# Kernel optimization log

Measured on AMD Instinct MI355X. Metric: run time of the kernel, lower is better.

## Reference

```python
import jax, jax.numpy as jnp
import numpy as np

B, N, C = 8192, 4, 768          # B = batch*tokens, N = n_streams, C = dim
HID = 4 * C                      # FFN hidden
EPS_RMS = 1.1920929e-7           # torch.finfo(float32).eps (nn.RMSNorm default eps=None)
EPS_SK = 1e-6                    # sinkhorn eps
SK_ITERS = 20
ALPHA = 0.01


def setup_inputs() -> dict:
    key = jax.random.key(0)
    ks = jax.random.split(key, 7)
    w = lambda k, shape: (jax.random.normal(k, shape, jnp.float32) * 0.02)
    return {
        "x": jax.random.normal(ks[0], (B, N, C), jnp.float32),
        "norm_w": jnp.ones((N * C,), jnp.float32),
        "w_pre": w(ks[1], (N, N * C)),
        "b_pre": jnp.zeros((N,), jnp.float32),
        "w_post": w(ks[2], (N, N * C)),
        "b_post": jnp.zeros((N,), jnp.float32),
        "w_res": w(ks[3], (N * N, N * C)),
        "b_res": jnp.zeros((N * N,), jnp.float32),
        "alpha_pre": jnp.array(ALPHA, jnp.float32),
        "alpha_post": jnp.array(ALPHA, jnp.float32),
        "alpha_res": jnp.array(ALPHA, jnp.float32),
        "w1": w(ks[4], (HID, C)),   # torch Linear weight layout [out, in]
        "b1": jnp.zeros((HID,), jnp.float32),
        "w2": w(ks[5], (C, HID)),
        "b2": jnp.zeros((C,), jnp.float32),
    }


def sinkhorn_knopp(logits):
    # logits: [B, n, n] -> doubly-stochastic matrix via 20 row/col normalizations
    M0 = jnp.exp(logits)

    def body(_, M):
        M = M / (M.sum(axis=-1, keepdims=True) + EPS_SK)
        M = M / (M.sum(axis=-2, keepdims=True) + EPS_SK)
        return M

    return jax.lax.fori_loop(0, SK_ITERS, body, M0)


def reference(x, norm_w, w_pre, b_pre, w_post, b_post, w_res, b_res,
              alpha_pre, alpha_post, alpha_res, w1, b1, w2, b2):
    b, n, c = x.shape
    x_flat = x.reshape(b, n * c)
    # RMSNorm over flattened streams
    x_norm = x_flat * jax.lax.rsqrt(jnp.mean(x_flat * x_flat, axis=-1, keepdims=True) + EPS_RMS) * norm_w
    # gate logits
    pre = alpha_pre * (x_norm @ w_pre.T) + b_pre            # [B, n]
    post = alpha_post * (x_norm @ w_post.T) + b_post        # [B, n]
    res_logits = (alpha_res * (x_norm @ w_res.T) + b_res).reshape(b, n, n)
    H_pre = jax.nn.sigmoid(pre)
    H_post = 2.0 * jax.nn.sigmoid(post)
    H_res = sinkhorn_knopp(res_logits)                      # [B, n, n]
    # pre-gate + stream mixing
    x_pre = x * H_pre[..., None]                            # [B, n, C]
    x_streams = jnp.einsum('bij,bjc->bic', H_res, x_pre)
    # fn = FFN applied on [B*n, C]
    h = jax.nn.gelu(x_streams.reshape(b * n, c) @ w1.T + b1, approximate=False)
    y = (h @ w2.T + b2).reshape(b, n, c)
    y = y * H_post[..., None]
    # residual mixed by the same DSM
    res = jnp.einsum('bij,bjc->bic', H_res, x)
    return res + y
```

## Files before the change

### kernel.cpp

```cpp
#include <hip/hip_runtime.h>

#define EPS_RMS 1.1920929e-7f
#define EPS_SK  1e-6f

typedef __bf16 bf16;
typedef __bf16 bf16x4 __attribute__((ext_vector_type(4)));
typedef __bf16 bf16x8 __attribute__((ext_vector_type(8)));
typedef float  f32x4  __attribute__((ext_vector_type(4)));

typedef __attribute__((address_space(3))) void lds_void;
typedef __attribute__((address_space(1))) void glb_void;

__device__ __forceinline__ void async_copy16(void* lds_dst, const void* gsrc) {
  __builtin_amdgcn_global_load_lds((glb_void*)gsrc, (lds_void*)lds_dst, 16, 0, 0);
}

__device__ __forceinline__ void wait_vmcnt0() {
  asm volatile("s_waitcnt vmcnt(0)" ::: "memory");
}

__device__ __forceinline__ void xcd_swizzle(int& bx, int& by) {
  const int gx = gridDim.x, nwg = gx * gridDim.y;
  const int flat = blockIdx.y * gx + blockIdx.x;
  const int q = nwg >> 3, r = nwg & 7;
  const int xcd = flat & 7, i = flat >> 3;
  const int lin = (xcd < r ? xcd * (q + 1) : r * (q + 1) + (xcd - r) * q) + i;
  bx = lin % gx;
  by = lin / gx;
}

__global__ __launch_bounds__(256) void convert_w_kernel(
    const float* __restrict__ w1, const float* __restrict__ w2,
    bf16* __restrict__ w1b, bf16* __restrict__ w2b) {
  size_t i = ((size_t)blockIdx.x * 256 + threadIdx.x) * 4;
  f32x4 a = *(const f32x4*)(w1 + i);
  f32x4 b = *(const f32x4*)(w2 + i);
  bf16x4 ab, bb;
#pragma unroll
  for (int q = 0; q < 4; ++q) { ab[q] = (bf16)a[q]; bb[q] = (bf16)b[q]; }
  *(bf16x4*)(w1b + i) = ab;
  *(bf16x4*)(w2b + i) = bb;
}

__global__ __launch_bounds__(256) void prep_wnb_kernel(
    const float* __restrict__ w_pre, const float* __restrict__ w_post,
    const float* __restrict__ w_res, const float* __restrict__ norm_w,
    bf16* __restrict__ wnb) {
  const int i = (blockIdx.x * 256 + threadIdx.x) * 4;
  const int j = i / 3072, k = i - j * 3072;
  f32x4 wv;
  if (j < 24) {
    const float* src = j < 4 ? (w_pre + j * 3072)
                     : (j < 8 ? (w_post + (j - 4) * 3072) : (w_res + (j - 8) * 3072));
    const f32x4 nv = *(const f32x4*)(norm_w + k);
    wv = *(const f32x4*)(src + k);
    wv = wv * nv;
  } else {
    wv = f32x4{0.f, 0.f, 0.f, 0.f};
  }
  bf16x4 o;
#pragma unroll
  for (int q = 0; q < 4; ++q) o[q] = (bf16)wv[q];
  *(bf16x4*)(wnb + i) = o;
}

__global__ __launch_bounds__(256) void gates_kernel(
    const float* __restrict__ x, const bf16* __restrict__ wnb,
    const float* __restrict__ b_pre, const float* __restrict__ b_post,
    const float* __restrict__ b_res,
    const float* __restrict__ alpha_pre, const float* __restrict__ alpha_post,
    const float* __restrict__ alpha_res, float* __restrict__ gates,
    bf16* __restrict__ xs, bf16* __restrict__ resb) {
  const int t = threadIdx.x, wv = t >> 6, l = t & 63;
  const int r0 = blockIdx.x * 16;
  __shared__ float buf[4][16][32];
  __shared__ float bsq[4][16];
  __shared__ float gm[16][20];

  f32x4 acc[2] = {};
  float sq = 0.f;
  const int kbase = wv * 768;
  const size_t arow = (size_t)(r0 + (l & 15)) * 3072;
  const int koff = (l >> 4) * 8;
#pragma unroll 1
  for (int ks = 0; ks < 24; ++ks) {
    const int k0 = kbase + ks * 32 + koff;
    const f32x4 a0 = *(const f32x4*)(x + arow + k0);
    const f32x4 a1 = *(const f32x4*)(x + arow + k0 + 4);
    sq += a0[0]*a0[0] + a0[1]*a0[1] + a0[2]*a0[2] + a0[3]*a0[3]
        + a1[0]*a1[0] + a1[1]*a1[1] + a1[2]*a1[2] + a1[3]*a1[3];
    bf16x8 af;
#pragma unroll
    for (int e = 0; e < 4; ++e) { af[e] = (bf16)a0[e]; af[4 + e] = (bf16)a1[e]; }
#pragma unroll
    for (int nf = 0; nf < 2; ++nf) {
      const bf16x8 bn = *(const bf16x8*)(wnb + (size_t)(nf * 16 + (l & 15)) * 3072 + k0);
      acc[nf] = __builtin_amdgcn_mfma_f32_16x16x32_bf16(af, bn, acc[nf], 0, 0, 0);
    }
  }
  sq += __shfl_xor(sq, 16);
  sq += __shfl_xor(sq, 32);
#pragma unroll
  for (int nf = 0; nf < 2; ++nf)
#pragma unroll
    for (int j = 0; j < 4; ++j)
      buf[wv][(l >> 4) * 4 + j][nf * 16 + (l & 15)] = acc[nf][j];
  if (l < 16) bsq[wv][l] = sq;
  __syncthreads();

  if (t < 16) {
    const int r = t;
    float dv[24];
#pragma unroll
    for (int j = 0; j < 24; ++j)
      dv[j] = buf[0][r][j] + buf[1][r][j] + buf[2][r][j] + buf[3][r][j];
    const float ssq = bsq[0][r] + bsq[1][r] + bsq[2][r] + bsq[3][r];
    const float rms = rsqrtf(ssq * (1.f / 3072.f) + EPS_RMS);
    const float ap = alpha_pre[0], apo = alpha_post[0], ar = alpha_res[0];
    float* g = gates + (size_t)(r0 + r) * 24;
    float M[16];
    float hp[4];
#pragma unroll
    for (int j = 0; j < 4; ++j) {
      const float p = ap * rms * dv[j] + b_pre[j];
      hp[j] = 1.f / (1.f + __expf(-p));
      g[j] = hp[j];
      const float q = apo * rms * dv[4 + j] + b_post[j];
      g[4 + j] = 2.f / (1.f + __expf(-q));
    }
#pragma unroll
    for (int j = 0; j < 16; ++j) M[j] = __expf(ar * rms * dv[8 + j] + b_res[j]);
    for (int it = 0; it < 20; ++it) {
#pragma unroll
      for (int i = 0; i < 4; ++i) {
        const float s = M[i * 4] + M[i * 4 + 1] + M[i * 4 + 2] + M[i * 4 + 3] + EPS_SK;
        const float ri = __fdividef(1.f, s);
#pragma unroll
        for (int j = 0; j < 4; ++j) M[i * 4 + j] *= ri;
      }
#pragma unroll
      for (int j = 0; j < 4; ++j) {
        const float s = M[j] + M[4 + j] + M[8 + j] + M[12 + j] + EPS_SK;
        const float ri = __fdividef(1.f, s);
#pragma unroll
        for (int i = 0; i < 4; ++i) M[i * 4 + j] *= ri;
      }
    }
#pragma unroll
    for (int j = 0; j < 16; ++j) { g[8 + j] = M[j]; gm[r][j] = M[j]; }
#pragma unroll
    for (int j = 0; j < 4; ++j) gm[r][16 + j] = hp[j];
  }
  __syncthreads();

  const int bb = t >> 4, tt = t & 15;
  float mr[4][4], mp[4][4];
#pragma unroll
  for (int i = 0; i < 4; ++i)
#pragma unroll
    for (int j = 0; j < 4; ++j) {
      mr[i][j] = gm[bb][i * 4 + j];
      mp[i][j] = mr[i][j] * gm[bb][16 + j];
    }
  const size_t xb = (size_t)(r0 + bb) * 3072;
#pragma unroll 1
  for (int cc = 0; cc < 12; ++cc) {
    const int c4 = (tt + cc * 16) * 4;
    f32x4 xj[4];
#pragma unroll
    for (int j = 0; j < 4; ++j)
      xj[j] = *(const f32x4*)(x + xb + (size_t)j * 768 + c4);
#pragma unroll
    for (int i = 0; i < 4; ++i) {
      f32x4 vr = mr[i][0] * xj[0] + mr[i][1] * xj[1] + mr[i][2] * xj[2] + mr[i][3] * xj[3];
      f32x4 vs = mp[i][0] * xj[0] + mp[i][1] * xj[1] + mp[i][2] * xj[2] + mp[i][3] * xj[3];
      bf16x4 ro, so;
#pragma unroll
      for (int q = 0; q < 4; ++q) { ro[q] = (bf16)vr[q]; so[q] = (bf16)vs[q]; }
      *(bf16x4*)(resb + xb + (size_t)i * 768 + c4) = ro;
      *(bf16x4*)(xs   + xb + (size_t)i * 768 + c4) = so;
    }
  }
}

__device__ __forceinline__ void gemm128_core(
    const bf16* __restrict__ A, const bf16* __restrict__ B, const int K,
    const int tM, const int tN, char* AL, char* BL, f32x4 (&acc)[4][4]) {
  const int t = threadIdx.x, l = t & 63, w = t >> 6;
  const int wr = w >> 1, wc = w & 1;
  const int NT = K >> 6;
  const int arow = wr * 64 + (l & 15);
  const int brow = wc * 64 + (l & 15);
  const int cb = l >> 4;

  auto frag = [&](const char* base, int row, int ks) -> bf16x8 {
    const int c = ks * 4 + cb;
    return *(const bf16x8*)(base + row * 128 + ((c ^ (row & 7)) << 4));
  };

  const int r0 = t >> 3;
  const int c0s = (t & 7) ^ (r0 & 7);
  const bf16* as0 = A + (size_t)(tM +      r0) * K + c0s * 8;
  const bf16* as1 = A + (size_t)(tM + 32 + r0) * K + c0s * 8;
  const bf16* as2 = A + (size_t)(tM + 64 + r0) * K + c0s * 8;
  const bf16* as3 = A + (size_t)(tM + 96 + r0) * K + c0s * 8;
  const bf16* bs0 = B + (size_t)(tN +      r0) * K + c0s * 8;
  const bf16* bs1 = B + (size_t)(tN + 32 + r0) * K + c0s * 8;
  const bf16* bs2 = B + (size_t)(tN + 64 + r0) * K + c0s * 8;
  const bf16* bs3 = B + (size_t)(tN + 96 + r0) * K + c0s * 8;
  char* ad0 = AL + t * 16;
  char* ad1 = AL + t * 16 + 4096;
  char* ad2 = AL + 8192 + t * 16;
  char* ad3 = AL + 8192 + t * 16 + 4096;
  char* bd0 = BL + t * 16;
  char* bd1 = BL + t * 16 + 4096;
  char* bd2 = BL + 8192 + t * 16;
  char* bd3 = BL + 8192 + t * 16 + 4096;

#pragma unroll 1
  for (int T = 0; T < NT; ++T) {
    async_copy16(ad0, as0); async_copy16(ad1, as1);
    async_copy16(bd0, bs0); async_copy16(bd1, bs1);
    async_copy16(ad2, as2); async_copy16(ad3, as3);
    async_copy16(bd2, bs2); async_copy16(bd3, bs3);
    as0 += 64; as1 += 64; as2 += 64; as3 += 64;
    bs0 += 64; bs1 += 64; bs2 += 64; bs3 += 64;
    wait_vmcnt0();
    __builtin_amdgcn_s_barrier();
#pragma unroll
    for (int ks = 0; ks < 2; ++ks) {
      bf16x8 af[4], bv[4];
#pragma unroll
      for (int mi = 0; mi < 4; ++mi) af[mi] = frag(AL, arow + mi * 16, ks);
#pragma unroll
      for (int ni = 0; ni < 4; ++ni) bv[ni] = frag(BL, brow + ni * 16, ks);
#pragma unroll
      for (int mi = 0; mi < 4; ++mi)
#pragma unroll
        for (int ni = 0; ni < 4; ++ni)
          acc[mi][ni] = __builtin_amdgcn_mfma_f32_16x16x32_bf16(af[mi], bv[ni], acc[mi][ni], 0, 0, 0);
    }
    __builtin_amdgcn_s_barrier();
  }
}

__global__ __launch_bounds__(256, 3) void ffn1_kernel(
    const bf16* __restrict__ xs, const bf16* __restrict__ w1b,
    const float* __restrict__ b1, bf16* __restrict__ h) {
  __shared__ __align__(16) char LDS[32768];
  int bx, by; xcd_swizzle(bx, by);
  const int tM = by * 128, tN = bx * 128;
  f32x4 acc[4][4] = {};
  gemm128_core(xs, w1b, 768, tM, tN, LDS, LDS + 16384, acc);

  const int t = threadIdx.x, l = t & 63;
  const int w = t >> 6, wr = w >> 1, wc = w & 1;
  float bias[4];
#pragma unroll
  for (int ni = 0; ni < 4; ++ni) bias[ni] = b1[tN + wc * 64 + ni * 16 + (l & 15)];

  __syncthreads();
  float* wlds = (float*)(LDS + w * 8192);
#pragma unroll
  for (int mi = 0; mi < 4; ++mi) {
#pragma unroll
    for (int j = 0; j < 4; ++j) {
      const int r = (l >> 4) * 4 + j;
#pragma unroll
      for (int ni = 0; ni < 4; ++ni) {
        const float v = acc[mi][ni][j] + bias[ni];
        const float y2 = 1.5957691216f * (v + 0.044715f * v * v * v);
        wlds[r * 68 + ni * 16 + (l & 15)] = __fdividef(v, 1.f + __expf(-y2));
      }
    }
    const int rr = l >> 3, c0 = (l & 7) * 8;
#pragma unroll
    for (int half = 0; half < 2; ++half) {
      const int row = rr + half * 8;
      const f32x4 u0 = *(const f32x4*)(wlds + row * 68 + c0);
      const f32x4 u1 = *(const f32x4*)(wlds + row * 68 + c0 + 4);
      bf16x8 ov;
#pragma unroll
      for (int q = 0; q < 4; ++q) { ov[q] = (bf16)u0[q]; ov[4 + q] = (bf16)u1[q]; }
      *(bf16x8*)(h + (size_t)(tM + wr * 64 + mi * 16 + row) * 3072 + tN + wc * 64 + c0) = ov;
    }
  }
}

__global__ __launch_bounds__(256, 3) void ffn2_kernel(
    const bf16* __restrict__ h, const bf16* __restrict__ w2b,
    const float* __restrict__ b2, const float* __restrict__ gates,
    const bf16* __restrict__ resb, float* __restrict__ outp, const int m0) {
  __shared__ __align__(16) char LDS[32768];
  int bx, by; xcd_swizzle(bx, by);
  const int tM = by * 128, tN = bx * 128;
  f32x4 acc[4][4] = {};
  gemm128_core(h, w2b, 3072, tM, tN, LDS, LDS + 16384, acc);

  const int t = threadIdx.x, l = t & 63;
  const int w = t >> 6, wr = w >> 1, wc = w & 1;
  float bias[4];
#pragma unroll
  for (int ni = 0; ni < 4; ++ni) bias[ni] = b2[tN + wc * 64 + ni * 16 + (l & 15)];

  __syncthreads();
  float* wlds = (float*)(LDS + w * 8192);
#pragma unroll
  for (int mi = 0; mi < 4; ++mi) {
#pragma unroll
    for (int j = 0; j < 4; ++j) {
      const int r = (l >> 4) * 4 + j;
#pragma unroll
      for (int ni = 0; ni < 4; ++ni)
        wlds[r * 68 + ni * 16 + (l & 15)] = acc[mi][ni][j] + bias[ni];
    }
#pragma unroll
    for (int rep = 0; rep < 4; ++rep) {
      const int row = rep * 4 + (l >> 4);
      const int cs = l & 15;
      const int mG = m0 + tM + wr * 64 + mi * 16 + row;
      const float hp = gates[(size_t)(mG >> 2) * 24 + 4 + (mG & 3)];
      const f32x4 v = *(const f32x4*)(wlds + row * 68 + cs * 4);
      const bf16x4 rb = *(const bf16x4*)(resb + (size_t)mG * 768 + tN + wc * 64 + cs * 4);
      f32x4 o;
#pragma unroll
      for (int q = 0; q < 4; ++q) o[q] = (float)rb[q] + v[q] * hp;
      *(f32x4*)(outp + (size_t)mG * 768 + tN + wc * 64 + cs * 4) = o;
    }
  }
}

extern "C" void kernel_launch(void* const* d_in, const int* in_sizes, int n_in,
                              void* d_out, int out_size, void* d_ws, size_t ws_size,
                              hipStream_t stream) {
  (void)in_sizes; (void)n_in; (void)out_size;
  const float* x         = (const float*)d_in[0];
  const float* norm_w    = (const float*)d_in[1];
  const float* w_pre     = (const float*)d_in[2];
  const float* b_pre     = (const float*)d_in[3];
  const float* w_post    = (const float*)d_in[4];
  const float* b_post    = (const float*)d_in[5];
  const float* w_res     = (const float*)d_in[6];
  const float* b_res     = (const float*)d_in[7];
  const float* alpha_pre = (const float*)d_in[8];
  const float* alpha_post= (const float*)d_in[9];
  const float* alpha_res = (const float*)d_in[10];
  const float* w1        = (const float*)d_in[11];
  const float* b1        = (const float*)d_in[12];
  const float* w2        = (const float*)d_in[13];
  const float* b2        = (const float*)d_in[14];
  float* outp = (float*)d_out;

  char* ws = (char*)d_ws;
  float* gates = (float*)ws;
  bf16*  w1b   = (bf16*)(ws + 786432);
  bf16*  w2b   = (bf16*)(ws + 5505024);
  bf16*  xs    = (bf16*)(ws + 10223616);
  bf16*  resb  = (bf16*)(ws + 60555264);
  bf16*  wnb   = (bf16*)(ws + 110886912);
  bf16*  h     = (bf16*)(ws + 111083520);

  size_t avail = ws_size > 111083520 ? ws_size - 111083520 : 0;
  long hrows = (long)(avail / (3072 * 2));
  hrows = (hrows / 256) * 256;
  if (hrows > 16384) hrows = 16384;
  if (hrows < 256) hrows = 256;

  convert_w_kernel<<<dim3(2304), dim3(256), 0, stream>>>(w1, w2, w1b, w2b);
  prep_wnb_kernel<<<dim3(96), dim3(256), 0, stream>>>(w_pre, w_post, w_res, norm_w, wnb);
  gates_kernel<<<dim3(512), dim3(256), 0, stream>>>(
      x, wnb, b_pre, b_post, b_res, alpha_pre, alpha_post, alpha_res, gates, xs, resb);

  for (long mo = 0; mo < 32768; mo += hrows) {
    const long mm = (32768 - mo) < hrows ? (32768 - mo) : hrows;
    ffn1_kernel<<<dim3(24, (unsigned)(mm / 128)), dim3(256), 0, stream>>>(
        xs + mo * 768, w1b, b1, h);
    ffn2_kernel<<<dim3(6, (unsigned)(mm / 128)), dim3(256), 0, stream>>>(
        h, w2b, b2, gates, resb, outp, (int)mo);
  }
}
```

Baseline: 442.0 us.

## Overlap FFN2 of first half with FFN1 of second half in one fused launch

Folds the weight bf16 conversion into the gates kernel as extra blocks, so one launch does both. When the workspace can hold h for all rows, the FFN is split into two halves. A mid kernel interleaves FFN2 tiles of the first half with FFN1 tiles of the second half in one grid, which fills the tail and drops launch gaps. This needs twice the h buffer and mixes two GEMM shapes in one grid, which may change cache behaviour.

```diff
diff --git a/kernel.cpp b/kernel.cpp
--- a/kernel.cpp
+++ b/kernel.cpp
@@ -19,27 +19,12 @@
   asm volatile("s_waitcnt vmcnt(0)" ::: "memory");
 }
 
-__device__ __forceinline__ void xcd_swizzle(int& bx, int& by) {
-  const int gx = gridDim.x, nwg = gx * gridDim.y;
-  const int flat = blockIdx.y * gx + blockIdx.x;
+__device__ __forceinline__ void swz_map(int flat, int nwg, int gx, int& bx, int& by) {
   const int q = nwg >> 3, r = nwg & 7;
   const int xcd = flat & 7, i = flat >> 3;
   const int lin = (xcd < r ? xcd * (q + 1) : r * (q + 1) + (xcd - r) * q) + i;
   bx = lin % gx;
   by = lin / gx;
-}
-
-__global__ __launch_bounds__(256) void convert_w_kernel(
-    const float* __restrict__ w1, const float* __restrict__ w2,
-    bf16* __restrict__ w1b, bf16* __restrict__ w2b) {
-  size_t i = ((size_t)blockIdx.x * 256 + threadIdx.x) * 4;
-  f32x4 a = *(const f32x4*)(w1 + i);
-  f32x4 b = *(const f32x4*)(w2 + i);
-  bf16x4 ab, bb;
-#pragma unroll
-  for (int q = 0; q < 4; ++q) { ab[q] = (bf16)a[q]; bb[q] = (bf16)b[q]; }
-  *(bf16x4*)(w1b + i) = ab;
-  *(bf16x4*)(w2b + i) = bb;
 }
 
 __global__ __launch_bounds__(256) void prep_wnb_kernel(
@@ -64,15 +49,30 @@
   *(bf16x4*)(wnb + i) = o;
 }
 
-__global__ __launch_bounds__(256) void gates_kernel(
+__global__ __launch_bounds__(256) void prep_fused_kernel(
     const float* __restrict__ x, const bf16* __restrict__ wnb,
     const float* __restrict__ b_pre, const float* __restrict__ b_post,
     const float* __restrict__ b_res,
     const float* __restrict__ alpha_pre, const float* __restrict__ alpha_post,
     const float* __restrict__ alpha_res, float* __restrict__ gates,
-    bf16* __restrict__ xs, bf16* __restrict__ resb) {
-  const int t = threadIdx.x, wv = t >> 6, l = t & 63;
-  const int r0 = blockIdx.x * 16;
+    bf16* __restrict__ xs, bf16* __restrict__ resb,
+    const float* __restrict__ w1, const float* __restrict__ w2,
+    bf16* __restrict__ w1b, bf16* __restrict__ w2b) {
+  const int fb = blockIdx.x;
+  const int t = threadIdx.x;
+  if (fb >= 512) {
+    size_t i = ((size_t)(fb - 512) * 256 + t) * 4;
+    f32x4 a = *(const f32x4*)(w1 + i);
+    f32x4 b = *(const f32x4*)(w2 + i);
+    bf16x4 ab, bb;
+#pragma unroll
+    for (int q = 0; q < 4; ++q) { ab[q] = (bf16)a[q]; bb[q] = (bf16)b[q]; }
+    *(bf16x4*)(w1b + i) = ab;
+    *(bf16x4*)(w2b + i) = bb;
+    return;
+  }
+  const int wv = t >> 6, l = t & 63;
+  const int r0 = fb * 16;
   __shared__ float buf[4][16][32];
   __shared__ float bsq[4][16];
   __shared__ float gm[16][20];
@@ -244,11 +244,10 @@
   }
 }
 
-__global__ __launch_bounds__(256, 3) void ffn1_kernel(
+__device__ __forceinline__ void ffn1_body(
     const bf16* __restrict__ xs, const bf16* __restrict__ w1b,
-    const float* __restrict__ b1, bf16* __restrict__ h) {
-  __shared__ __align__(16) char LDS[32768];
-  int bx, by; xcd_swizzle(bx, by);
+    const float* __restrict__ b1, bf16* __restrict__ h,
+    const int bx, const int by, char* LDS) {
   const int tM = by * 128, tN = bx * 128;
   f32x4 acc[4][4] = {};
   gemm128_core(xs, w1b, 768, tM, tN, LDS, LDS + 16384, acc);
@@ -287,12 +286,11 @@
   }
 }
 
-__global__ __launch_bounds__(256, 3) void ffn2_kernel(
+__device__ __forceinline__ void ffn2_body(
     const bf16* __restrict__ h, const bf16* __restrict__ w2b,
     const float* __restrict__ b2, const float* __restrict__ gates,
-    const bf16* __restrict__ resb, float* __restrict__ outp, const int m0) {
-  __shared__ __align__(16) char LDS[32768];
-  int bx, by; xcd_swizzle(bx, by);
+    const bf16* __restrict__ resb, float* __restrict__ outp, const int m0,
+    const int bx, const int by, char* LDS) {
   const int tM = by * 128, tN = bx * 128;
   f32x4 acc[4][4] = {};
   gemm128_core(h, w2b, 3072, tM, tN, LDS, LDS + 16384, acc);
@@ -327,6 +325,43 @@
       for (int q = 0; q < 4; ++q) o[q] = (float)rb[q] + v[q] * hp;
       *(f32x4*)(outp + (size_t)mG * 768 + tN + wc * 64 + cs * 4) = o;
     }
+  }
+}
+
+__global__ __launch_bounds__(256, 3) void ffn1_kernel(
+    const bf16* __restrict__ xs, const bf16* __restrict__ w1b,
+    const float* __restrict__ b1, bf16* __restrict__ h) {
+  __shared__ __align__(16) char LDS[32768];
+  int bx, by; swz_map(blockIdx.x, gridDim.x, 24, bx, by);
+  ffn1_body(xs, w1b, b1, h, bx, by, LDS);
+}
+
+__global__ __launch_bounds__(256, 3) void ffn2_kernel(
+    const bf16* __restrict__ h, const bf16* __restrict__ w2b,
+    const float* __restrict__ b2, const float* __restrict__ gates,
+    const bf16* __restrict__ resb, float* __restrict__ outp, const int m0) {
+  __shared__ __align__(16) char LDS[32768];
+  int bx, by; swz_map(blockIdx.x, gridDim.x, 6, bx, by);
+  ffn2_body(h, w2b, b2, gates, resb, outp, m0, bx, by, LDS);
+}
+
+__global__ __launch_bounds__(256, 3) void mid_fused_kernel(
+    const bf16* __restrict__ xs2, const bf16* __restrict__ w1b,
+    const float* __restrict__ b1, bf16* __restrict__ h2,
+    const bf16* __restrict__ h1, const bf16* __restrict__ w2b,
+    const float* __restrict__ b2, const float* __restrict__ gates,
+    const bf16* __restrict__ resb, float* __restrict__ outp) {
+  __shared__ __align__(16) char LDS[32768];
+  const int flat = blockIdx.x;
+  const int grp = flat % 5;
+  if (grp == 4) {
+    const int idx = flat / 5;
+    int bx, by; swz_map(idx, 768, 6, bx, by);
+    ffn2_body(h1, w2b, b2, gates, resb, outp, 0, bx, by, LDS);
+  } else {
+    const int idx = (flat / 5) * 4 + grp;
+    int bx, by; swz_map(idx, 3072, 24, bx, by);
+    ffn1_body(xs2, w1b, b1, h2, bx, by, LDS);
   }
 }
 
@@ -363,19 +398,31 @@
   size_t avail = ws_size > 111083520 ? ws_size - 111083520 : 0;
   long hrows = (long)(avail / (3072 * 2));
   hrows = (hrows / 256) * 256;
-  if (hrows > 16384) hrows = 16384;
+  if (hrows > 32768) hrows = 32768;
   if (hrows < 256) hrows = 256;
 
-  convert_w_kernel<<<dim3(2304), dim3(256), 0, stream>>>(w1, w2, w1b, w2b);
   prep_wnb_kernel<<<dim3(96), dim3(256), 0, stream>>>(w_pre, w_post, w_res, norm_w, wnb);
-  gates_kernel<<<dim3(512), dim3(256), 0, stream>>>(
-      x, wnb, b_pre, b_post, b_res, alpha_pre, alpha_post, alpha_res, gates, xs, resb);
-
-  for (long mo = 0; mo < 32768; mo += hrows) {
-    const long mm = (32768 - mo) < hrows ? (32768 - mo) : hrows;
-    ffn1_kernel<<<dim3(24, (unsigned)(mm / 128)), dim3(256), 0, stream>>>(
-        xs + mo * 768, w1b, b1, h);
-    ffn2_kernel<<<dim3(6, (unsigned)(mm / 128)), dim3(256), 0, stream>>>(
-        h, w2b, b2, gates, resb, outp, (int)mo);
-  }
-}
+  prep_fused_kernel<<<dim3(2816), dim3(256), 0, stream>>>(
+      x, wnb, b_pre, b_post, b_res, alpha_pre, alpha_post, alpha_res, gates, xs, resb,
+      w1, w2, w1b, w2b);
+
+  if (hrows >= 32768) {
+    const long c = 16384;
+    ffn1_kernel<<<dim3(24 * (unsigned)(c / 128)), dim3(256), 0, stream>>>(
+        xs, w1b, b1, h);
+    mid_fused_kernel<<<dim3(3840), dim3(256), 0, stream>>>(
+        xs + c * 768, w1b, b1, h + c * 3072,
+        h, w2b, b2, gates, resb, outp);
+    ffn2_kernel<<<dim3(6 * (unsigned)(c / 128)), dim3(256), 0, stream>>>(
+        h + c * 3072, w2b, b2, gates, resb, outp, (int)c);
+  } else {
+    if (hrows > 16384) hrows = 16384;
+    for (long mo = 0; mo < 32768; mo += hrows) {
+      const long mm = (32768 - mo) < hrows ? (32768 - mo) : hrows;
+      ffn1_kernel<<<dim3(24 * (unsigned)(mm / 128)), dim3(256), 0, stream>>>(
+          xs + mo * 768, w1b, b1, h);
+      ffn2_kernel<<<dim3(6 * (unsigned)(mm / 128)), dim3(256), 0, stream>>>(
+          h, w2b, b2, gates, resb, outp, (int)mo);
+    }
+  }
+}
```

Measured after the change: 514.1 us. 16.3% more time.
